# Kernel optimization log

Measured on AMD Instinct MI355X. Metric: run time of the kernel, lower is better.

The kernel has to match this reference:

```python
import jax, jax.numpy as jnp
import numpy as np

B, N, D = 8, 256, 16   # batch, set size, in_dim
HID = 256              # hidden width (hidden_dims[:-1])
H = 128                # attention feature dim (hidden_dims[-1])
DH = 64                # per-dim feature dim d_h
NH = 4                 # attention heads


def _made_masks():
    in_deg = np.arange(1, D + 1)
    h_deg = (np.arange(HID) % (D - 1)) + 1
    out_deg = np.repeat(in_deg, H)  # per-dim contiguous layout -> reshape(..., D, H)
    m0 = h_deg[None, :] >= in_deg[:, None]
    m1 = h_deg[None, :] >= h_deg[:, None]
    m2 = out_deg[None, :] > h_deg[:, None]
    return jnp.array(m0), jnp.array(m1), jnp.array(m2)


def setup_inputs() -> dict:
    key = jax.random.key(0)
    ks = iter(jax.random.split(key, 40))
    def w(fi, fo):
        return jax.random.normal(next(ks), (fi, fo), jnp.float32) / np.sqrt(fi)
    inp = {"t": jnp.array([0.5], jnp.float32),
           "x": jax.random.normal(next(ks), (B, N, D), jnp.float32)}
    qd = [D, HID, HID, H * D]
    kd = [D, HID, HID, H]
    dd = [DH + 2, HID, HID, H, 1]
    for i in range(3):
        inp[f"q_w{i}"] = w(qd[i], qd[i + 1]); inp[f"q_b{i}"] = jnp.zeros((qd[i + 1],), jnp.float32)
        inp[f"k_w{i}"] = w(kd[i], kd[i + 1]); inp[f"k_b{i}"] = jnp.zeros((kd[i + 1],), jnp.float32)
        inp[f"v_w{i}"] = w(kd[i], kd[i + 1]); inp[f"v_b{i}"] = jnp.zeros((kd[i + 1],), jnp.float32)
    inp["p_w"] = w(H, DH); inp["p_b"] = jnp.zeros((DH,), jnp.float32)
    for i in range(4):
        inp[f"d_w{i}"] = w(dd[i], dd[i + 1]); inp[f"d_b{i}"] = jnp.zeros((dd[i + 1],), jnp.float32)
    inp["q_m0"], inp["q_m1"], inp["q_m2"] = _made_masks()
    return inp


def reference(t, x, q_w0, q_b0, k_w0, k_b0, v_w0, v_b0, q_w1, q_b1, k_w1, k_b1, v_w1, v_b1,
              q_w2, q_b2, k_w2, k_b2, v_w2, v_b2, p_w, p_b,
              d_w0, d_b0, d_w1, d_b1, d_w2, d_b2, d_w3, d_b3, q_m0, q_m1, q_m2):
    # --- exclusive net: MADE query (hollow per dim), MLP key/value, diagonal-masked attention ---
    hq = jax.nn.relu(x @ (q_w0 * q_m0) + q_b0)
    hq = jax.nn.relu(hq @ (q_w1 * q_m1) + q_b1)
    q = (hq @ (q_w2 * q_m2) + q_b2).reshape(B, N, D, H)      # [B,N,D,H]

    def mlp3(z, w0, b0, w1, b1, w2, b2):
        z = jnp.tanh(z @ w0 + b0)
        z = jnp.tanh(z @ w1 + b1)
        return z @ w2 + b2

    k = mlp3(x, k_w0, k_b0, k_w1, k_b1, k_w2, k_b2)          # [B,N,H] (shared across dims)
    v = mlp3(x, v_w0, v_b0, v_w1, v_b1, v_w2, v_b2)          # [B,N,H]

    dh = H // NH
    qh = q.transpose(0, 2, 1, 3).reshape(B, D, N, NH, dh).transpose(0, 1, 3, 2, 4)  # [B,D,NH,N,dh]
    kh = k.reshape(B, N, NH, dh).transpose(0, 2, 1, 3)        # [B,NH,N,dh]
    vh = v.reshape(B, N, NH, dh).transpose(0, 2, 1, 3)

    # einsum avoids materializing the repeat_interleaved key/value (same math)
    scores = jnp.einsum('bdhnc,bhmc->bdhnm', qh, kh) / np.sqrt(dh)
    scores = jnp.where(jnp.eye(N, dtype=bool), -jnp.inf, scores)  # mask self-attention (hollow)
    att = jax.nn.softmax(scores, axis=-1)
    o = jnp.einsum('bdhnm,bhmc->bdhnc', att, vh)              # [B,D,NH,N,dh]
    o = o.transpose(0, 1, 3, 2, 4).reshape(B, D, N, H).transpose(0, 2, 1, 3)  # [B,N,D,H]
    hfeat = o @ p_w + p_b                                     # [B,N,D,DH], hollow wrt x[...,d]

    # --- dimwise net: y_d = MLP([t, x_d, h_d]); exact diagonal Jacobian via jvp on x channel ---
    tb = jnp.broadcast_to(t.reshape(()), (B, N, D, 1)).astype(x.dtype)
    def dimwise(xc):
        z = jnp.concatenate([tb, xc, hfeat], -1)              # [B,N,D,2+DH]
        z = jnp.tanh(z @ d_w0 + d_b0)
        z = jnp.tanh(z @ d_w1 + d_b1)
        z = jnp.tanh(z @ d_w2 + d_b2)
        return (z @ d_w3 + d_b3)[..., 0]                      # [B,N,D]

    y, jac = jax.jvp(dimwise, (x[..., None],), (jnp.ones((B, N, D, 1), x.dtype),))
    return y, jac
```

## Files before the change

kernel.cpp:

```cpp
#include <hip/hip_runtime.h>
#include <hip/hip_bf16.h>

constexpr int kB = 8, kN = 256, kD = 16, kHID = 256, kH = 128, kDH = 64, kdh = 32;
constexpr int kBN = kB * kN;
constexpr int kP  = kBN * kD;

__device__ __forceinline__ float b2f(__hip_bfloat16 v) { return __bfloat162float(v); }
__device__ __forceinline__ __hip_bfloat16 f2b(float v) { return __float2bfloat16(v); }
__device__ __forceinline__ unsigned short f2bs(float v) {
    __hip_bfloat16 h = __float2bfloat16(v);
    return *(unsigned short*)&h;
}

__device__ __forceinline__ float tanh_fast(float v) {
    float e = __expf(2.f * v);
    return 1.f - 2.f * __builtin_amdgcn_rcpf(e + 1.f);
}

typedef short s8v  __attribute__((ext_vector_type(8)));
typedef float f4v  __attribute__((ext_vector_type(4)));
#define MFMA(a, b, c) __builtin_amdgcn_mfma_f32_16x16x32_bf16((a), (b), (c), 0, 0, 0)

__global__ __launch_bounds__(256) void prep_frag(
    const float* p_w, const float* d_w0, const float* d_w1, const float* d_w2,
    const float* k_w0, const float* k_w1, const float* k_w2,
    const float* v_w0, const float* v_w1, const float* v_w2,
    const float* q_w0, const float* q_w1, const float* q_w2,
    __hip_bfloat16* pwf, __hip_bfloat16* w0f, __hip_bfloat16* w1f, __hip_bfloat16* w2f,
    __hip_bfloat16* k0f, __hip_bfloat16* k1f, __hip_bfloat16* k2f,
    __hip_bfloat16* v0f, __hip_bfloat16* v1f, __hip_bfloat16* v2f,
    __hip_bfloat16* q0f, __hip_bfloat16* q1f, __hip_bfloat16* q2f)
{
    const int tile = blockIdx.x * 4 + (threadIdx.x >> 6);
    const int lane = threadIdx.x & 63;
    const float* src; __hip_bfloat16* dst; int N, NT, local, Kreal = 1 << 30, mask = 0;
    if (tile < 16)        { src = p_w;        dst = pwf; N = 64;   NT = 4;   local = tile; }
    else if (tile < 48)   { src = d_w0 + 512; dst = w0f; N = 256;  NT = 16;  local = tile - 16; }
    else if (tile < 176)  { src = d_w1;       dst = w1f; N = 256;  NT = 16;  local = tile - 48; }
    else if (tile < 240)  { src = d_w2;       dst = w2f; N = 128;  NT = 8;   local = tile - 176; }
    else if (tile < 256)  { src = k_w0;       dst = k0f; N = 256;  NT = 16;  local = tile - 240; Kreal = 16; }
    else if (tile < 272)  { src = v_w0;       dst = v0f; N = 256;  NT = 16;  local = tile - 256; Kreal = 16; }
    else if (tile < 288)  { src = q_w0;       dst = q0f; N = 256;  NT = 16;  local = tile - 272; Kreal = 16; mask = 1; }
    else if (tile < 416)  { src = k_w1;       dst = k1f; N = 256;  NT = 16;  local = tile - 288; }
    else if (tile < 544)  { src = v_w1;       dst = v1f; N = 256;  NT = 16;  local = tile - 416; }
    else if (tile < 672)  { src = q_w1;       dst = q1f; N = 256;  NT = 16;  local = tile - 544; mask = 2; }
    else if (tile < 736)  { src = k_w2;       dst = k2f; N = 128;  NT = 8;   local = tile - 672; }
    else if (tile < 800)  { src = v_w2;       dst = v2f; N = 128;  NT = 8;   local = tile - 736; }
    else                  { src = q_w2;       dst = q2f; N = 2048; NT = 128; local = tile - 800; mask = 3; }
    const int kt = local / NT, nt = local % NT;
    const int row0 = kt * 32 + (lane >> 4) * 8;
    const int col  = nt * 16 + (lane & 15);
    __hip_bfloat16* o = dst + ((size_t)local * 64 + lane) * 8;
    #pragma unroll
    for (int j = 0; j < 8; ++j) {
        const int r = row0 + j;
        float w = (r < Kreal) ? src[(size_t)r * N + col] : 0.f;
        if (mask == 1 && !((col % 15) >= r))        w = 0.f;
        if (mask == 2 && !((col % 15) >= (r % 15))) w = 0.f;
        if (mask == 3 && !((col >> 7) > (r % 15)))  w = 0.f;
        o[j] = f2b(w);
    }
}

__global__ __launch_bounds__(256) void mlp_kernel(
    const float* x,
    const float* k_b0, const float* k_b1, const float* k_b2,
    const float* v_b0, const float* v_b1, const float* v_b2,
    const float* q_b0, const float* q_b1,
    const __hip_bfloat16* k0f, const __hip_bfloat16* k1f, const __hip_bfloat16* k2f,
    const __hip_bfloat16* v0f, const __hip_bfloat16* v1f, const __hip_bfloat16* v2f,
    const __hip_bfloat16* q0f, const __hip_bfloat16* q1f,
    __hip_bfloat16* kbuf, __hip_bfloat16* vbuf, __hip_bfloat16* h1q)
{
    constexpr int SA = 264;
    constexpr int SX = 40;
    __shared__ __hip_bfloat16 xin[32 * SX];
    __shared__ __hip_bfloat16 bufA[32 * SA];
    __shared__ __hip_bfloat16 bufB[32 * SA];

    const int tid  = threadIdx.x;
    const int wv   = tid >> 6, lane = tid & 63;
    const int lx   = lane & 15, quad = lane >> 4;
    const int path = blockIdx.x >> 6;
    const int r0   = (blockIdx.x & 63) * 32;

    auto ldA = [&](const __hip_bfloat16* buf, int stride, int m0, int k0) -> s8v {
        return *(const s8v*)(buf + (m0 + lx) * stride + k0 + quad * 8);
    };
    auto ldB = [&](const __hip_bfloat16* wf, int NT, int kt, int nt) -> s8v {
        return *(const s8v*)(wf + (((size_t)(kt * NT + nt) * 64 + lane) << 3));
    };

    for (int idx = tid; idx < 1024; idx += 256) {
        const int row = idx >> 5, c = idx & 31;
        xin[row * SX + c] = f2b(c < 16 ? x[(r0 + row) * kD + c] : 0.f);
    }

    const __hip_bfloat16* F0[3] = { k0f, v0f, q0f };
    const __hip_bfloat16* F1[3] = { k1f, v1f, q1f };
    const __hip_bfloat16* F2[2] = { k2f, v2f };
    const float* Ba0[3] = { k_b0, v_b0, q_b0 };
    const float* Ba1[3] = { k_b1, v_b1, q_b1 };
    const float* Ba2[2] = { k_b2, v_b2 };
    __hip_bfloat16* O2[2] = { kbuf, vbuf };

    __syncthreads();

    {
        f4v acc[4][2] = {};
        const s8v a0 = ldA(xin, SX, 0, 0);
        const s8v a1 = ldA(xin, SX, 16, 0);
        #pragma unroll
        for (int j = 0; j < 4; ++j) {
            s8v b = ldB(F0[path], 16, 0, wv * 4 + j);
            acc[j][0] = MFMA(a0, b, acc[j][0]);
            acc[j][1] = MFMA(a1, b, acc[j][1]);
        }
        #pragma unroll
        for (int j = 0; j < 4; ++j) {
            const int n = (wv * 4 + j) * 16 + lx;
            const float bb = Ba0[path][n];
            #pragma unroll
            for (int mt = 0; mt < 2; ++mt)
            #pragma unroll
            for (int r = 0; r < 4; ++r) {
                const float v = acc[j][mt][r] + bb;
                const float z = (path == 2) ? fmaxf(v, 0.f) : tanh_fast(v);
                bufA[(mt * 16 + quad * 4 + r) * SA + n] = f2b(z);
            }
        }
    }
    __syncthreads();

    {
        f4v acc[4][2] = {};
        #pragma unroll
        for (int kt = 0; kt < 8; ++kt) {
            const s8v a0 = ldA(bufA, SA, 0, kt * 32);
            const s8v a1 = ldA(bufA, SA, 16, kt * 32);
            #pragma unroll
            for (int j = 0; j < 4; ++j) {
                s8v b = ldB(F1[path], 16, kt, wv * 4 + j);
                acc[j][0] = MFMA(a0, b, acc[j][0]);
                acc[j][1] = MFMA(a1, b, acc[j][1]);
            }
        }
        #pragma unroll
        for (int j = 0; j < 4; ++j) {
            const int n = (wv * 4 + j) * 16 + lx;
            const float bb = Ba1[path][n];
            #pragma unroll
            for (int mt = 0; mt < 2; ++mt)
            #pragma unroll
            for (int r = 0; r < 4; ++r) {
                const int m = mt * 16 + quad * 4 + r;
                const float v = acc[j][mt][r] + bb;
                if (path == 2) {
                    h1q[(size_t)(r0 + m) * 256 + n] = f2b(fmaxf(v, 0.f));
                } else {
                    bufB[m * SA + n] = f2b(tanh_fast(v));
                }
            }
        }
    }
    if (path == 2) return;
    __syncthreads();

    {
        f4v acc[2][2] = {};
        #pragma unroll
        for (int kt = 0; kt < 8; ++kt) {
            const s8v a0 = ldA(bufB, SA, 0, kt * 32);
            const s8v a1 = ldA(bufB, SA, 16, kt * 32);
            #pragma unroll
            for (int j = 0; j < 2; ++j) {
                s8v b = ldB(F2[path], 8, kt, wv * 2 + j);
                acc[j][0] = MFMA(a0, b, acc[j][0]);
                acc[j][1] = MFMA(a1, b, acc[j][1]);
            }
        }
        #pragma unroll
        for (int j = 0; j < 2; ++j) {
            const int n = (wv * 2 + j) * 16 + lx;
            const float bb = Ba2[path][n];
            #pragma unroll
            for (int mt = 0; mt < 2; ++mt)
            #pragma unroll
            for (int r = 0; r < 4; ++r) {
                const int m = mt * 16 + quad * 4 + r;
                O2[path][(size_t)(r0 + m) * kH + n] = f2b(acc[j][mt][r] + bb);
            }
        }
    }
}

__global__ __launch_bounds__(256) void qgemm_kernel(
    const float* q_b2, const __hip_bfloat16* h1q, const __hip_bfloat16* q2f,
    __hip_bfloat16* qbuf)
{
    constexpr int SA = 264;
    __shared__ __hip_bfloat16 hin[32 * SA];

    const int tid  = threadIdx.x;
    const int wv   = tid >> 6, lane = tid & 63;
    const int lx   = lane & 15, quad = lane >> 4;
    const int ct   = blockIdx.x & 7;
    const int r0   = (blockIdx.x >> 3) * 32;

    for (int idx = tid; idx < 1024; idx += 256) {
        const int row = idx >> 5, seg = idx & 31;
        *(f4v*)(hin + row * SA + seg * 8) = *(const f4v*)(h1q + (size_t)(r0 + row) * 256 + seg * 8);
    }
    __syncthreads();

    f4v acc[4][2] = {};
    #pragma unroll
    for (int kt = 0; kt < 8; ++kt) {
        const s8v a0 = *(const s8v*)(hin + lx * SA + kt * 32 + quad * 8);
        const s8v a1 = *(const s8v*)(hin + (16 + lx) * SA + kt * 32 + quad * 8);
        #pragma unroll
        for (int j = 0; j < 4; ++j) {
            s8v b = *(const s8v*)(q2f + (((size_t)(kt * 128 + ct * 16 + wv * 4 + j) * 64 + lane) << 3));
            acc[j][0] = MFMA(a0, b, acc[j][0]);
            acc[j][1] = MFMA(a1, b, acc[j][1]);
        }
    }
    const float scale = 0.17677669529663687f;
    #pragma unroll
    for (int j = 0; j < 4; ++j) {
        const int col = ct * 256 + (wv * 4 + j) * 16 + lx;
        const float bb = q_b2[col];
        #pragma unroll
        for (int mt = 0; mt < 2; ++mt)
        #pragma unroll
        for (int r = 0; r < 4; ++r) {
            const int row = r0 + mt * 16 + quad * 4 + r;
            qbuf[(size_t)row * 2048 + col] = f2b((acc[j][mt][r] + bb) * scale);
        }
    }
}

__global__ __launch_bounds__(256, 2) void attn_kernel(
    const __hip_bfloat16* qbuf, const __hip_bfloat16* kbuf, const __hip_bfloat16* vbuf,
    __hip_bfloat16* obuf)
{
    constexpr int SP = 264;
    __shared__ short Pl[4][16 * SP];

    const int blk = blockIdx.x;
    const int hd = blk & 3;
    const int d  = (blk >> 2) & 15;
    const int b  = blk >> 6;

    const int wv   = threadIdx.x >> 6;
    const int lane = threadIdx.x & 63;
    const int lx = lane & 15, quad = lane >> 4;
    short* Pw = &Pl[wv][0];

    const short* kb = (const short*)kbuf;
    const short* vb = (const short*)vbuf;
    const short* qb = (const short*)qbuf;

    s8v kfrag[16];
    #pragma unroll
    for (int mt = 0; mt < 16; ++mt)
        kfrag[mt] = *(const s8v*)(kb + (size_t)(b * 256 + mt * 16 + lx) * 128 + hd * 32 + quad * 8);

    s8v vfrag[2][8];
    #pragma unroll
    for (int ntv = 0; ntv < 2; ++ntv)
    #pragma unroll
    for (int kt = 0; kt < 8; ++kt) {
        s8v v;
        #pragma unroll
        for (int j = 0; j < 8; ++j)
            v[j] = vb[(size_t)(b * 256 + kt * 32 + quad * 8 + j) * 128 + hd * 32 + ntv * 16 + lx];
        vfrag[ntv][kt] = v;
    }

    const float LOG2E = 1.4426950408889634f;

    for (int mi = 0; mi < 4; ++mi) {
        const int q0 = wv * 64 + mi * 16;

        s8v qfrag = *(const s8v*)(qb + (size_t)(b * 256 + q0 + lx) * 2048 + d * 128 + hd * 32 + quad * 8);

        f4v acc[16];
        #pragma unroll
        for (int mt = 0; mt < 16; ++mt) acc[mt] = f4v{0.f, 0.f, 0.f, 0.f};
        #pragma unroll
        for (int mt = 0; mt < 16; ++mt) acc[mt] = MFMA(kfrag[mt], qfrag, acc[mt]);

        const int qg = q0 + lx;
        float mx = -3.0e38f;
        #pragma unroll
        for (int mt = 0; mt < 16; ++mt)
        #pragma unroll
        for (int r = 0; r < 4; ++r) {
            const int key = mt * 16 + quad * 4 + r;
            float s = (key == qg) ? -3.0e38f : acc[mt][r];
            acc[mt][r] = s;
            mx = fmaxf(mx, s);
        }
        mx = fmaxf(mx, __shfl_xor(mx, 16, 64));
        mx = fmaxf(mx, __shfl_xor(mx, 32, 64));

        const float nmxc = -mx * LOG2E;
        float l = 0.f;
        #pragma unroll
        for (int mt = 0; mt < 16; ++mt)
        #pragma unroll
        for (int r = 0; r < 4; ++r) {
            float p = exp2f(__builtin_fmaf(acc[mt][r], LOG2E, nmxc));
            acc[mt][r] = p;
            l += p;
        }
        l += __shfl_xor(l, 16, 64);
        l += __shfl_xor(l, 32, 64);

        #pragma unroll
        for (int mt = 0; mt < 16; ++mt) {
            unsigned short h0 = f2bs(acc[mt][0]);
            unsigned short h1 = f2bs(acc[mt][1]);
            unsigned short h2 = f2bs(acc[mt][2]);
            unsigned short h3 = f2bs(acc[mt][3]);
            uint2 w;
            w.x = (unsigned int)h0 | ((unsigned int)h1 << 16);
            w.y = (unsigned int)h2 | ((unsigned int)h3 << 16);
            *(uint2*)(Pw + lx * SP + mt * 16 + quad * 4) = w;
        }
        __asm__ volatile("s_waitcnt lgkmcnt(0)" ::: "memory");

        f4v av[2] = { f4v{0.f,0.f,0.f,0.f}, f4v{0.f,0.f,0.f,0.f} };
        #pragma unroll
        for (int kt = 0; kt < 8; ++kt) {
            s8v a = *(const s8v*)(Pw + lx * SP + kt * 32 + quad * 8);
            av[0] = MFMA(a, vfrag[0][kt], av[0]);
            av[1] = MFMA(a, vfrag[1][kt], av[1]);
        }
        __asm__ volatile("s_waitcnt lgkmcnt(0)" ::: "memory");

        #pragma unroll
        for (int r = 0; r < 4; ++r) {
            const float lr = __shfl(l, quad * 4 + r, 64);
            const float inv = __builtin_amdgcn_rcpf(lr);
            const int qrow = q0 + quad * 4 + r;
            #pragma unroll
            for (int ntv = 0; ntv < 2; ++ntv) {
                obuf[((size_t)((b * 256 + qrow) * 16 + d)) * 128 + hd * 32 + ntv * 16 + lx]
                    = f2b(av[ntv][r] * inv);
            }
        }
    }
}

__global__ __launch_bounds__(256) void dim_kernel(
    const float* t, const float* x,
    const float* p_b, const float* d_w0, const float* d_b0,
    const float* d_b1, const float* d_b2, const float* d_w3, const float* d_b3,
    const __hip_bfloat16* pwf, const __hip_bfloat16* w0f,
    const __hip_bfloat16* w1f, const __hip_bfloat16* w2f,
    const __hip_bfloat16* obuf, float* out)
{
    constexpr int SA = 264;
    constexpr int SO = 136;
    constexpr int SH = 72;
    __shared__ __hip_bfloat16 bufA[32 * SA];
    __shared__ __hip_bfloat16 bufB[32 * SA];
    __shared__ __hip_bfloat16 bufH[16 * SH];
    __shared__ float xvs[16];

    const int tid  = threadIdx.x;
    const int wv   = tid >> 6, lane = tid & 63;
    const int lx   = lane & 15, quad = lane >> 4;
    const int p0   = blockIdx.x * 16;
    const float tval = t[0];

    auto ldA = [&](const __hip_bfloat16* buf, int stride, int m0, int k0) -> s8v {
        return *(const s8v*)(buf + (m0 + lx) * stride + k0 + quad * 8);
    };
    auto ldBf = [&](const __hip_bfloat16* wf, int NT, int kt, int nt) -> s8v {
        return *(const s8v*)(wf + (((size_t)(kt * NT + nt) * 64 + lane) << 3));
    };

    for (int idx = tid; idx < 256; idx += 256) {
        const int row = idx >> 4, ch = idx & 15;
        *(f4v*)(bufA + row * SO + ch * 8) = *(const f4v*)(obuf + (size_t)(p0 + row) * kH + ch * 8);
    }
    if (tid < 16) xvs[tid] = x[p0 + tid];
    __syncthreads();

    {
        f4v acc0 = {};
        #pragma unroll
        for (int ktile = 0; ktile < 4; ++ktile) {
            s8v b  = ldBf(pwf, 4, ktile, wv);
            s8v a0 = ldA(bufA, SO, 0, ktile * 32);
            acc0 = MFMA(a0, b, acc0);
        }
        const int n = wv * 16 + lx;
        const float bb = p_b[n];
        #pragma unroll
        for (int r = 0; r < 4; ++r)
            bufH[(quad * 4 + r) * SH + n] = f2b(acc0[r] + bb);
    }
    __syncthreads();

    {
        f4v acc[4] = {};
        #pragma unroll
        for (int ktile = 0; ktile < 2; ++ktile) {
            s8v a0 = ldA(bufH, SH, 0, ktile * 32);
            #pragma unroll
            for (int j = 0; j < 4; ++j) {
                s8v b = ldBf(w0f, 16, ktile, wv * 4 + j);
                acc[j] = MFMA(a0, b, acc[j]);
            }
        }
        #pragma unroll
        for (int j = 0; j < 4; ++j) {
            const int n = (wv * 4 + j) * 16 + lx;
            const float base = d_b0[n] + tval * d_w0[n];
            const float wx   = d_w0[256 + n];
            #pragma unroll
            for (int r = 0; r < 4; ++r) {
                const int m = quad * 4 + r;
                const float z = tanh_fast(acc[j][r] + base + xvs[m] * wx);
                bufB[m * SA + n]        = f2b(z);
                bufB[(m + 16) * SA + n] = f2b((1.f - z * z) * wx);
            }
        }
    }
    __syncthreads();

    {
        f4v acc[4][2] = {};
        #pragma unroll
        for (int ktile = 0; ktile < 8; ++ktile) {
            s8v a0 = ldA(bufB, SA, 0,  ktile * 32);
            s8v a1 = ldA(bufB, SA, 16, ktile * 32);
            #pragma unroll
            for (int j = 0; j < 4; ++j) {
                s8v b = ldBf(w1f, 16, ktile, wv * 4 + j);
                acc[j][0] = MFMA(a0, b, acc[j][0]);
                acc[j][1] = MFMA(a1, b, acc[j][1]);
            }
        }
        #pragma unroll
        for (int j = 0; j < 4; ++j) {
            const int n = (wv * 4 + j) * 16 + lx;
            const float b1 = d_b1[n];
            #pragma unroll
            for (int r = 0; r < 4; ++r) {
                const int m = quad * 4 + r;
                const float z  = tanh_fast(acc[j][0][r] + b1);
                const float zd = (1.f - z * z) * acc[j][1][r];
                bufA[m * SA + n]        = f2b(z);
                bufA[(m + 16) * SA + n] = f2b(zd);
            }
        }
    }
    __syncthreads();

    {
        f4v acc[2][2] = {};
        #pragma unroll
        for (int ktile = 0; ktile < 8; ++ktile) {
            s8v a0 = ldA(bufA, SA, 0,  ktile * 32);
            s8v a1 = ldA(bufA, SA, 16, ktile * 32);
            #pragma unroll
            for (int j = 0; j < 2; ++j) {
                s8v b = ldBf(w2f, 8, ktile, wv * 2 + j);
                acc[j][0] = MFMA(a0, b, acc[j][0]);
                acc[j][1] = MFMA(a1, b, acc[j][1]);
            }
        }
        #pragma unroll
        for (int j = 0; j < 2; ++j) {
            const int n = (wv * 2 + j) * 16 + lx;
            const float b2 = d_b2[n];
            #pragma unroll
            for (int r = 0; r < 4; ++r) {
                const int m = quad * 4 + r;
                const float z  = tanh_fast(acc[j][0][r] + b2);
                const float zd = (1.f - z * z) * acc[j][1][r];
                bufB[m * SO + n]        = f2b(z);
                bufB[(m + 16) * SO + n] = f2b(zd);
            }
        }
    }
    __syncthreads();

    {
        const int p = tid >> 4, s = tid & 15;
        float yv = 0.f, jv = 0.f;
        #pragma unroll
        for (int i = 0; i < 8; ++i) {
            const int n = s + i * 16;
            const float w = d_w3[n];
            yv += b2f(bufB[p * SO + n]) * w;
            jv += b2f(bufB[(p + 16) * SO + n]) * w;
        }
        #pragma unroll
        for (int off = 8; off > 0; off >>= 1) {
            yv += __shfl_down(yv, off, 16);
            jv += __shfl_down(jv, off, 16);
        }
        if (s == 0) {
            out[p0 + p]      = yv + d_b3[0];
            out[kP + p0 + p] = jv;
        }
    }
}

extern "C" void kernel_launch(void* const* d_in, const int* in_sizes, int n_in,
                              void* d_out, int out_size, void* d_ws, size_t ws_size,
                              hipStream_t stream)
{
    typedef const float* fp;
    fp t    = (fp)d_in[0];
    fp x    = (fp)d_in[1];
    fp q_w0 = (fp)d_in[2],  q_b0 = (fp)d_in[3];
    fp k_w0 = (fp)d_in[4],  k_b0 = (fp)d_in[5];
    fp v_w0 = (fp)d_in[6],  v_b0 = (fp)d_in[7];
    fp q_w1 = (fp)d_in[8],  q_b1 = (fp)d_in[9];
    fp k_w1 = (fp)d_in[10], k_b1 = (fp)d_in[11];
    fp v_w1 = (fp)d_in[12], v_b1 = (fp)d_in[13];
    fp q_w2 = (fp)d_in[14], q_b2 = (fp)d_in[15];
    fp k_w2 = (fp)d_in[16], k_b2 = (fp)d_in[17];
    fp v_w2 = (fp)d_in[18], v_b2 = (fp)d_in[19];
    fp p_w  = (fp)d_in[20], p_b  = (fp)d_in[21];
    fp d_w0 = (fp)d_in[22], d_b0 = (fp)d_in[23];
    fp d_w1 = (fp)d_in[24], d_b1 = (fp)d_in[25];
    fp d_w2 = (fp)d_in[26], d_b2 = (fp)d_in[27];
    fp d_w3 = (fp)d_in[28], d_b3 = (fp)d_in[29];

    __hip_bfloat16* wsb  = (__hip_bfloat16*)d_ws;
    __hip_bfloat16* kbuf = wsb;
    __hip_bfloat16* vbuf = kbuf + (size_t)kBN * kH;
    __hip_bfloat16* qbuf = vbuf + (size_t)kBN * kH;
    __hip_bfloat16* obuf = qbuf + (size_t)kBN * kD * kH;
    __hip_bfloat16* pwf  = obuf + (size_t)kP * kH;
    __hip_bfloat16* w0f  = pwf + 8192;
    __hip_bfloat16* w1f  = w0f + 16384;
    __hip_bfloat16* w2f  = w1f + 65536;
    __hip_bfloat16* k0f  = w2f + 32768;
    __hip_bfloat16* v0f  = k0f + 8192;
    __hip_bfloat16* q0f  = v0f + 8192;
    __hip_bfloat16* k1f  = q0f + 8192;
    __hip_bfloat16* v1f  = k1f + 65536;
    __hip_bfloat16* q1f  = v1f + 65536;
    __hip_bfloat16* k2f  = q1f + 65536;
    __hip_bfloat16* v2f  = k2f + 32768;
    __hip_bfloat16* q2f  = v2f + 32768;
    __hip_bfloat16* h1q  = q2f + 524288;

    float* out = (float*)d_out;

    prep_frag<<<456, 256, 0, stream>>>(p_w, d_w0, d_w1, d_w2,
        k_w0, k_w1, k_w2, v_w0, v_w1, v_w2, q_w0, q_w1, q_w2,
        pwf, w0f, w1f, w2f, k0f, k1f, k2f, v0f, v1f, v2f, q0f, q1f, q2f);
    mlp_kernel<<<192, 256, 0, stream>>>(x,
        k_b0, k_b1, k_b2, v_b0, v_b1, v_b2, q_b0, q_b1,
        k0f, k1f, k2f, v0f, v1f, v2f, q0f, q1f, kbuf, vbuf, h1q);
    qgemm_kernel<<<(kBN / 32) * 8, 256, 0, stream>>>(q_b2, h1q, q2f, qbuf);
    attn_kernel<<<kB * kD * 4, 256, 0, stream>>>(qbuf, kbuf, vbuf, obuf);
    dim_kernel<<<kP / 16, 256, 0, stream>>>(t, x, p_b, d_w0, d_b0, d_b1, d_b2, d_w3, d_b3,
        pwf, w0f, w1f, w2f, obuf, out);
}
```

Measured before the change: 194.8 us.

## Fold projection weight into first dimwise layer and widen dim_kernel to 512 threads

Precomputes the product of the output projection p_w and the hfeat rows of d_w0 into one 128x256 bf16 weight, plus a folded bias. This removes the separate projection GEMM, its shared-memory staging buffer and one barrier from dim_kernel. dim_kernel also moves to 512 threads, so each wave computes fewer output columns per layer, and the final reduction uses 32-lane groups. The folding adds a small serial dot-product loop in the prep kernels and an extra launch, and it changes bf16 rounding because the intermediate hfeat is no longer rounded.

```diff
diff --git a/kernel.cpp b/kernel.cpp
--- a/kernel.cpp
+++ b/kernel.cpp
@@ -26,30 +26,45 @@
     const float* k_w0, const float* k_w1, const float* k_w2,
     const float* v_w0, const float* v_w1, const float* v_w2,
     const float* q_w0, const float* q_w1, const float* q_w2,
-    __hip_bfloat16* pwf, __hip_bfloat16* w0f, __hip_bfloat16* w1f, __hip_bfloat16* w2f,
+    __hip_bfloat16* wcf, __hip_bfloat16* w1f, __hip_bfloat16* w2f,
     __hip_bfloat16* k0f, __hip_bfloat16* k1f, __hip_bfloat16* k2f,
     __hip_bfloat16* v0f, __hip_bfloat16* v1f, __hip_bfloat16* v2f,
     __hip_bfloat16* q0f, __hip_bfloat16* q1f, __hip_bfloat16* q2f)
 {
     const int tile = blockIdx.x * 4 + (threadIdx.x >> 6);
     const int lane = threadIdx.x & 63;
+    const int lx = lane & 15, quad = lane >> 4;
+
+    if (tile < 64) {
+        const int kt = tile / 16, nt = tile % 16;
+        const int col = nt * 16 + lx;
+        __hip_bfloat16* o = wcf + ((size_t)tile * 64 + lane) * 8;
+        #pragma unroll
+        for (int j = 0; j < 8; ++j) {
+            const int row = kt * 32 + quad * 8 + j;
+            float s = 0.f;
+            for (int d = 0; d < 64; ++d)
+                s += p_w[row * 64 + d] * d_w0[(2 + d) * 256 + col];
+            o[j] = f2b(s);
+        }
+        return;
+    }
+
     const float* src; __hip_bfloat16* dst; int N, NT, local, Kreal = 1 << 30, mask = 0;
-    if (tile < 16)        { src = p_w;        dst = pwf; N = 64;   NT = 4;   local = tile; }
-    else if (tile < 48)   { src = d_w0 + 512; dst = w0f; N = 256;  NT = 16;  local = tile - 16; }
-    else if (tile < 176)  { src = d_w1;       dst = w1f; N = 256;  NT = 16;  local = tile - 48; }
-    else if (tile < 240)  { src = d_w2;       dst = w2f; N = 128;  NT = 8;   local = tile - 176; }
-    else if (tile < 256)  { src = k_w0;       dst = k0f; N = 256;  NT = 16;  local = tile - 240; Kreal = 16; }
-    else if (tile < 272)  { src = v_w0;       dst = v0f; N = 256;  NT = 16;  local = tile - 256; Kreal = 16; }
-    else if (tile < 288)  { src = q_w0;       dst = q0f; N = 256;  NT = 16;  local = tile - 272; Kreal = 16; mask = 1; }
-    else if (tile < 416)  { src = k_w1;       dst = k1f; N = 256;  NT = 16;  local = tile - 288; }
-    else if (tile < 544)  { src = v_w1;       dst = v1f; N = 256;  NT = 16;  local = tile - 416; }
-    else if (tile < 672)  { src = q_w1;       dst = q1f; N = 256;  NT = 16;  local = tile - 544; mask = 2; }
-    else if (tile < 736)  { src = k_w2;       dst = k2f; N = 128;  NT = 8;   local = tile - 672; }
-    else if (tile < 800)  { src = v_w2;       dst = v2f; N = 128;  NT = 8;   local = tile - 736; }
-    else                  { src = q_w2;       dst = q2f; N = 2048; NT = 128; local = tile - 800; mask = 3; }
+    if (tile < 192)       { src = d_w1; dst = w1f; N = 256;  NT = 16;  local = tile - 64; }
+    else if (tile < 256)  { src = d_w2; dst = w2f; N = 128;  NT = 8;   local = tile - 192; }
+    else if (tile < 272)  { src = k_w0; dst = k0f; N = 256;  NT = 16;  local = tile - 256; Kreal = 16; }
+    else if (tile < 288)  { src = v_w0; dst = v0f; N = 256;  NT = 16;  local = tile - 272; Kreal = 16; }
+    else if (tile < 304)  { src = q_w0; dst = q0f; N = 256;  NT = 16;  local = tile - 288; Kreal = 16; mask = 1; }
+    else if (tile < 432)  { src = k_w1; dst = k1f; N = 256;  NT = 16;  local = tile - 304; }
+    else if (tile < 560)  { src = v_w1; dst = v1f; N = 256;  NT = 16;  local = tile - 432; }
+    else if (tile < 688)  { src = q_w1; dst = q1f; N = 256;  NT = 16;  local = tile - 560; mask = 2; }
+    else if (tile < 752)  { src = k_w2; dst = k2f; N = 128;  NT = 8;   local = tile - 688; }
+    else if (tile < 816)  { src = v_w2; dst = v2f; N = 128;  NT = 8;   local = tile - 752; }
+    else                  { src = q_w2; dst = q2f; N = 2048; NT = 128; local = tile - 816; mask = 3; }
     const int kt = local / NT, nt = local % NT;
-    const int row0 = kt * 32 + (lane >> 4) * 8;
-    const int col  = nt * 16 + (lane & 15);
+    const int row0 = kt * 32 + quad * 8;
+    const int col  = nt * 16 + lx;
     __hip_bfloat16* o = dst + ((size_t)local * 64 + lane) * 8;
     #pragma unroll
     for (int j = 0; j < 8; ++j) {
@@ -62,6 +77,15 @@
     }
 }
 
+__global__ __launch_bounds__(256) void prep_bias(
+    const float* p_b, const float* d_w0, float* bc0)
+{
+    const int n = threadIdx.x;
+    float s = 0.f;
+    for (int d = 0; d < 64; ++d) s += p_b[d] * d_w0[(2 + d) * 256 + n];
+    bc0[n] = s;
+}
+
 __global__ __launch_bounds__(256) void mlp_kernel(
     const float* x,
     const float* k_b0, const float* k_b1, const float* k_b2,
@@ -354,20 +378,17 @@
     }
 }
 
-__global__ __launch_bounds__(256) void dim_kernel(
+__global__ __launch_bounds__(512) void dim_kernel(
     const float* t, const float* x,
-    const float* p_b, const float* d_w0, const float* d_b0,
+    const float* d_w0, const float* d_b0, const float* bc0,
     const float* d_b1, const float* d_b2, const float* d_w3, const float* d_b3,
-    const __hip_bfloat16* pwf, const __hip_bfloat16* w0f,
-    const __hip_bfloat16* w1f, const __hip_bfloat16* w2f,
+    const __hip_bfloat16* wcf, const __hip_bfloat16* w1f, const __hip_bfloat16* w2f,
     const __hip_bfloat16* obuf, float* out)
 {
     constexpr int SA = 264;
     constexpr int SO = 136;
-    constexpr int SH = 72;
     __shared__ __hip_bfloat16 bufA[32 * SA];
     __shared__ __hip_bfloat16 bufB[32 * SA];
-    __shared__ __hip_bfloat16 bufH[16 * SH];
     __shared__ float xvs[16];
 
     const int tid  = threadIdx.x;
@@ -383,44 +404,28 @@
         return *(const s8v*)(wf + (((size_t)(kt * NT + nt) * 64 + lane) << 3));
     };
 
-    for (int idx = tid; idx < 256; idx += 256) {
-        const int row = idx >> 4, ch = idx & 15;
+    if (tid < 256) {
+        const int row = tid >> 4, ch = tid & 15;
         *(f4v*)(bufA + row * SO + ch * 8) = *(const f4v*)(obuf + (size_t)(p0 + row) * kH + ch * 8);
     }
     if (tid < 16) xvs[tid] = x[p0 + tid];
     __syncthreads();
 
     {
-        f4v acc0 = {};
+        f4v acc[2] = {};
         #pragma unroll
         for (int ktile = 0; ktile < 4; ++ktile) {
-            s8v b  = ldBf(pwf, 4, ktile, wv);
             s8v a0 = ldA(bufA, SO, 0, ktile * 32);
-            acc0 = MFMA(a0, b, acc0);
-        }
-        const int n = wv * 16 + lx;
-        const float bb = p_b[n];
-        #pragma unroll
-        for (int r = 0; r < 4; ++r)
-            bufH[(quad * 4 + r) * SH + n] = f2b(acc0[r] + bb);
-    }
-    __syncthreads();
-
-    {
-        f4v acc[4] = {};
-        #pragma unroll
-        for (int ktile = 0; ktile < 2; ++ktile) {
-            s8v a0 = ldA(bufH, SH, 0, ktile * 32);
-            #pragma unroll
-            for (int j = 0; j < 4; ++j) {
-                s8v b = ldBf(w0f, 16, ktile, wv * 4 + j);
+            #pragma unroll
+            for (int j = 0; j < 2; ++j) {
+                s8v b = ldBf(wcf, 16, ktile, wv * 2 + j);
                 acc[j] = MFMA(a0, b, acc[j]);
             }
         }
         #pragma unroll
-        for (int j = 0; j < 4; ++j) {
-            const int n = (wv * 4 + j) * 16 + lx;
-            const float base = d_b0[n] + tval * d_w0[n];
+        for (int j = 0; j < 2; ++j) {
+            const int n = (wv * 2 + j) * 16 + lx;
+            const float base = bc0[n] + d_b0[n] + tval * d_w0[n];
             const float wx   = d_w0[256 + n];
             #pragma unroll
             for (int r = 0; r < 4; ++r) {
@@ -434,21 +439,21 @@
     __syncthreads();
 
     {
-        f4v acc[4][2] = {};
+        f4v acc[2][2] = {};
         #pragma unroll
         for (int ktile = 0; ktile < 8; ++ktile) {
             s8v a0 = ldA(bufB, SA, 0,  ktile * 32);
             s8v a1 = ldA(bufB, SA, 16, ktile * 32);
             #pragma unroll
-            for (int j = 0; j < 4; ++j) {
-                s8v b = ldBf(w1f, 16, ktile, wv * 4 + j);
+            for (int j = 0; j < 2; ++j) {
+                s8v b = ldBf(w1f, 16, ktile, wv * 2 + j);
                 acc[j][0] = MFMA(a0, b, acc[j][0]);
                 acc[j][1] = MFMA(a1, b, acc[j][1]);
             }
         }
         #pragma unroll
-        for (int j = 0; j < 4; ++j) {
-            const int n = (wv * 4 + j) * 16 + lx;
+        for (int j = 0; j < 2; ++j) {
+            const int n = (wv * 2 + j) * 16 + lx;
             const float b1 = d_b1[n];
             #pragma unroll
             for (int r = 0; r < 4; ++r) {
@@ -463,48 +468,42 @@
     __syncthreads();
 
     {
-        f4v acc[2][2] = {};
+        f4v acc[2] = {};
         #pragma unroll
         for (int ktile = 0; ktile < 8; ++ktile) {
             s8v a0 = ldA(bufA, SA, 0,  ktile * 32);
             s8v a1 = ldA(bufA, SA, 16, ktile * 32);
-            #pragma unroll
-            for (int j = 0; j < 2; ++j) {
-                s8v b = ldBf(w2f, 8, ktile, wv * 2 + j);
-                acc[j][0] = MFMA(a0, b, acc[j][0]);
-                acc[j][1] = MFMA(a1, b, acc[j][1]);
-            }
-        }
-        #pragma unroll
-        for (int j = 0; j < 2; ++j) {
-            const int n = (wv * 2 + j) * 16 + lx;
-            const float b2 = d_b2[n];
-            #pragma unroll
-            for (int r = 0; r < 4; ++r) {
-                const int m = quad * 4 + r;
-                const float z  = tanh_fast(acc[j][0][r] + b2);
-                const float zd = (1.f - z * z) * acc[j][1][r];
-                bufB[m * SO + n]        = f2b(z);
-                bufB[(m + 16) * SO + n] = f2b(zd);
-            }
-        }
-    }
-    __syncthreads();
-
-    {
-        const int p = tid >> 4, s = tid & 15;
+            s8v b = ldBf(w2f, 8, ktile, wv);
+            acc[0] = MFMA(a0, b, acc[0]);
+            acc[1] = MFMA(a1, b, acc[1]);
+        }
+        const int n = wv * 16 + lx;
+        const float b2 = d_b2[n];
+        #pragma unroll
+        for (int r = 0; r < 4; ++r) {
+            const int m = quad * 4 + r;
+            const float z  = tanh_fast(acc[0][r] + b2);
+            const float zd = (1.f - z * z) * acc[1][r];
+            bufB[m * SO + n]        = f2b(z);
+            bufB[(m + 16) * SO + n] = f2b(zd);
+        }
+    }
+    __syncthreads();
+
+    {
+        const int p = tid >> 5, s = tid & 31;
         float yv = 0.f, jv = 0.f;
         #pragma unroll
-        for (int i = 0; i < 8; ++i) {
-            const int n = s + i * 16;
+        for (int i = 0; i < 4; ++i) {
+            const int n = s + i * 32;
             const float w = d_w3[n];
             yv += b2f(bufB[p * SO + n]) * w;
             jv += b2f(bufB[(p + 16) * SO + n]) * w;
         }
         #pragma unroll
-        for (int off = 8; off > 0; off >>= 1) {
-            yv += __shfl_down(yv, off, 16);
-            jv += __shfl_down(jv, off, 16);
+        for (int off = 16; off > 0; off >>= 1) {
+            yv += __shfl_down(yv, off, 32);
+            jv += __shfl_down(jv, off, 32);
         }
         if (s == 0) {
             out[p0 + p]      = yv + d_b3[0];
@@ -540,9 +539,8 @@
     __hip_bfloat16* vbuf = kbuf + (size_t)kBN * kH;
     __hip_bfloat16* qbuf = vbuf + (size_t)kBN * kH;
     __hip_bfloat16* obuf = qbuf + (size_t)kBN * kD * kH;
-    __hip_bfloat16* pwf  = obuf + (size_t)kP * kH;
-    __hip_bfloat16* w0f  = pwf + 8192;
-    __hip_bfloat16* w1f  = w0f + 16384;
+    __hip_bfloat16* wcf  = obuf + (size_t)kP * kH;
+    __hip_bfloat16* w1f  = wcf + 32768;
     __hip_bfloat16* w2f  = w1f + 65536;
     __hip_bfloat16* k0f  = w2f + 32768;
     __hip_bfloat16* v0f  = k0f + 8192;
@@ -554,17 +552,19 @@
     __hip_bfloat16* v2f  = k2f + 32768;
     __hip_bfloat16* q2f  = v2f + 32768;
     __hip_bfloat16* h1q  = q2f + 524288;
+    float* bc0 = (float*)(h1q + 524288);
 
     float* out = (float*)d_out;
 
-    prep_frag<<<456, 256, 0, stream>>>(p_w, d_w0, d_w1, d_w2,
+    prep_frag<<<460, 256, 0, stream>>>(p_w, d_w0, d_w1, d_w2,
         k_w0, k_w1, k_w2, v_w0, v_w1, v_w2, q_w0, q_w1, q_w2,
-        pwf, w0f, w1f, w2f, k0f, k1f, k2f, v0f, v1f, v2f, q0f, q1f, q2f);
+        wcf, w1f, w2f, k0f, k1f, k2f, v0f, v1f, v2f, q0f, q1f, q2f);
+    prep_bias<<<1, 256, 0, stream>>>(p_b, d_w0, bc0);
     mlp_kernel<<<192, 256, 0, stream>>>(x,
         k_b0, k_b1, k_b2, v_b0, v_b1, v_b2, q_b0, q_b1,
         k0f, k1f, k2f, v0f, v1f, v2f, q0f, q1f, kbuf, vbuf, h1q);
     qgemm_kernel<<<(kBN / 32) * 8, 256, 0, stream>>>(q_b2, h1q, q2f, qbuf);
     attn_kernel<<<kB * kD * 4, 256, 0, stream>>>(qbuf, kbuf, vbuf, obuf);
-    dim_kernel<<<kP / 16, 256, 0, stream>>>(t, x, p_b, d_w0, d_b0, d_b1, d_b2, d_w3, d_b3,
-        pwf, w0f, w1f, w2f, obuf, out);
-}
+    dim_kernel<<<kP / 16, 512, 0, stream>>>(t, x, d_w0, d_b0, bc0,
+        d_b1, d_b2, d_w3, d_b3, wcf, w1f, w2f, obuf, out);
+}
```

Result: slower. 207.4 us (+6.4%).
